# Optimization experiments

Hardware: AMD Instinct MI355X
Metric: run time of the kernel (lower is better)

The kernel has to match this reference:

```python
import jax, jax.numpy as jnp
import numpy as np

MIN_, MAX_, KSZ, IGNORE_IDX = 10, 10, 3, -255
B, H, W = 256, 256, 256
LI_MAX_ITERS = 64


def setup_inputs() -> dict:
    key = jax.random.key(0)
    x = jax.random.uniform(key, (B, 1, H, W), dtype=jnp.float32)
    return {"x": x}


def _otsu(hist):
    # hist: [256] counts. Returns Otsu threshold (bin value); fg = img > t.
    bins = jnp.arange(256, dtype=jnp.float32)
    w0 = jnp.cumsum(hist)[:-1]
    w1 = hist.sum() - w0
    s0 = jnp.cumsum(hist * bins)[:-1]
    s_tot = (hist * bins).sum()
    m0 = s0 / jnp.maximum(w0, 1e-12)
    m1 = (s_tot - s0) / jnp.maximum(w1, 1e-12)
    var_b = w0 * w1 * (m0 - m1) ** 2
    return jnp.argmax(var_b).astype(jnp.float32)


def _li(hist, init_t):
    # Histogram-based Li iterative minimum cross-entropy threshold
    # (skimage.filters.threshold_li with initial_guess=init_t).
    bins = jnp.arange(256, dtype=jnp.float32)
    img_min = jnp.min(jnp.where(hist > 0, bins, 255.0))
    vals = bins - img_min  # shift so values >= 0 (as skimage does)
    csum = jnp.cumsum(hist)
    cvsum = jnp.cumsum(hist * vals)
    n_tot, s_tot = csum[-1], cvsum[-1]
    tol = 0.5  # integer image -> half the minimal value spacing

    def body(state):
        t_curr, _, i = state
        # background: img <= t_curr + img_min
        idx = jnp.clip(jnp.floor(t_curr + img_min).astype(jnp.int32), 0, 255)
        n_back, s_back = csum[idx], cvsum[idx]
        n_fore, s_fore = n_tot - n_back, s_tot - s_back
        mean_back = jnp.where(n_back > 0, s_back / jnp.maximum(n_back, 1.0), 0.0)
        mean_fore = s_fore / jnp.maximum(n_fore, 1.0)
        eps = 1e-12
        t_next = (mean_back - mean_fore) / (
            jnp.log(jnp.maximum(mean_back, eps)) - jnp.log(jnp.maximum(mean_fore, eps)))
        t_next = jnp.where(mean_back < eps, mean_fore / 2.0, t_next)
        return (t_next, t_curr, i + 1)

    def cond(state):
        t_curr, t_prev, i = state
        return (jnp.abs(t_curr - t_prev) > tol) & (i < LI_MAX_ITERS)

    t0 = init_t - img_min
    t_fin, _, _ = jax.lax.while_loop(cond, body, (t0, t0 + 10.0, 0))
    return t_fin + img_min


def _sample_mask(key, region, k):
    # Uniform sampling without replacement of up to k pixels from region
    # (bool [H,W]) via random-score top-k (equiv. to torch.multinomial
    # with uniform probs, w/o replacement).
    flat = region.reshape(-1)
    scores = jnp.where(flat, jax.random.uniform(key, (flat.shape[0],)), -1.0)
    top, idx = jax.lax.top_k(scores, k)
    valid = (top >= 0.0).astype(jnp.int32)
    mask = jnp.zeros(flat.shape[0], jnp.int32).at[idx].max(valid)
    return mask.reshape(region.shape)


def _dilate(m):
    # kornia dilation with ones (KSZ,KSZ) kernel on a 0/1 mask == max filter.
    return jax.lax.reduce_window(m, 0, jax.lax.max, (KSZ, KSZ), (1, 1), "SAME")


def _per_image(img_u8, key_fg, key_bg):
    # img_u8: [H,W] int32 in [0,255]
    hist = jnp.zeros(256, jnp.float32).at[img_u8.ravel()].add(1.0)
    otsu = jnp.clip(_otsu(hist), 1.0, 254.0)  # clamp 0->1, 255->254
    li_t = _li(hist, otsu)
    roi = img_u8.astype(jnp.float32) > li_t

    fg = _sample_mask(key_fg, roi, MAX_)
    bg = _sample_mask(key_bg, jnp.logical_not(roi), MIN_)
    if KSZ > 1:
        fg = _dilate(fg)
        bg = _dilate(bg)

    overlap = (fg + bg) == 2
    fg = jnp.where(overlap, 0, fg)
    bg = jnp.where(overlap, 0, bg)

    seeds = jnp.full((H, W), IGNORE_IDX, jnp.int32)
    seeds = jnp.where(bg == 1, 0, seeds)
    seeds = jnp.where(fg == 1, 1, seeds)
    return seeds


def reference(x):
    b = x.shape[0]
    # (cam*255).astype(uint8): truncation, cam in [0,1]
    img = jnp.clip(jnp.floor(x[:, 0] * 255.0), 0, 255).astype(jnp.int32)
    keys = jax.random.split(jax.random.key(1), (b, 2))
    return jax.vmap(_per_image)(img, keys[:, 0], keys[:, 1])
```

## Files before the change

kernel.cpp:

```cpp
#include <hip/hip_runtime.h>
#include <stdint.h>

#define NPIX 65536
#define IGN (-255)
#define CAP 768

__device__ __forceinline__ uint32_t rotl32(uint32_t v, uint32_t r){
  return __builtin_amdgcn_alignbit(v, v, 32u - r);
}

__device__ __forceinline__ void tf2x32(uint32_t k0, uint32_t k1, uint32_t x0, uint32_t x1,
                                       uint32_t &o0, uint32_t &o1){
  uint32_t k2 = k0 ^ k1 ^ 0x1BD11BDAu;
  x0 += k0; x1 += k1;
#define TFR(r) { x0 += x1; x1 = rotl32(x1,(r)); x1 ^= x0; }
  TFR(13u) TFR(15u) TFR(26u) TFR(6u)   x0 += k1; x1 += k2 + 1u;
  TFR(17u) TFR(29u) TFR(16u) TFR(24u)  x0 += k2; x1 += k0 + 2u;
  TFR(13u) TFR(15u) TFR(26u) TFR(6u)   x0 += k0; x1 += k1 + 3u;
  TFR(17u) TFR(29u) TFR(16u) TFR(24u)  x0 += k1; x1 += k2 + 4u;
  TFR(13u) TFR(15u) TFR(26u) TFR(6u)   x0 += k2; x1 += k0 + 5u;
#undef TFR
  o0 = x0; o1 = x1;
}

__device__ __forceinline__ void tf4_quad(
  uint32_t A0, uint32_t A1, uint32_t A2,
  uint32_t B0, uint32_t B1, uint32_t B2,
  uint32_t C0, uint32_t C1, uint32_t C2,
  uint32_t D0, uint32_t D1, uint32_t D2,
  uint32_t px,
  uint32_t &rA, uint32_t &rB, uint32_t &rC, uint32_t &rD)
{
  uint32_t a0 = A0, a1 = px + A1;
  uint32_t b0 = B0, b1 = (px + 1u) + B1;
  uint32_t c0 = C0, c1 = (px + 2u) + C1;
  uint32_t d0 = D0, d1 = (px + 3u) + D1;
#define R4(r) { a0 += a1; b0 += b1; c0 += c1; d0 += d1;                       \
  a1 = rotl32(a1,(r)); b1 = rotl32(b1,(r)); c1 = rotl32(c1,(r)); d1 = rotl32(d1,(r)); \
  a1 ^= a0; b1 ^= b0; c1 ^= c0; d1 ^= d0; }
#define INJ4(KA,KB,KC,KD, JA,JB,JC,JD, i) {                                   \
  a0 += (KA); b0 += (KB); c0 += (KC); d0 += (KD);                             \
  a1 += (JA) + (i); b1 += (JB) + (i); c1 += (JC) + (i); d1 += (JD) + (i); }
  R4(13u) R4(15u) R4(26u) R4(6u)
  INJ4(A1,B1,C1,D1, A2,B2,C2,D2, 1u)
  R4(17u) R4(29u) R4(16u) R4(24u)
  INJ4(A2,B2,C2,D2, A0,B0,C0,D0, 2u)
  R4(13u) R4(15u) R4(26u) R4(6u)
  INJ4(A0,B0,C0,D0, A1,B1,C1,D1, 3u)
  R4(17u) R4(29u) R4(16u) R4(24u)
  INJ4(A1,B1,C1,D1, A2,B2,C2,D2, 4u)
  R4(13u) R4(15u) R4(26u) R4(6u)
  INJ4(A2,B2,C2,D2, A0,B0,C0,D0, 5u)
#undef R4
#undef INJ4
  rA = a0 ^ a1; rB = b0 ^ b1; rC = c0 ^ c1; rD = d0 ^ d1;
}

__device__ __forceinline__ unsigned long long packCand(uint32_t bits, uint32_t pix){
  float f = __uint_as_float((bits >> 9) | 0x3f800000u) - 1.0f;
  uint32_t u = __float_as_uint(f) ^ 0x80000000u;
  return ((unsigned long long)u << 32) | (unsigned long long)(0xFFFFFFFFu - pix);
}

__device__ __forceinline__ void t10_insert(unsigned long long* l, unsigned long long c){
  if (c > l[9]) {
    l[9] = c;
#pragma unroll
    for (int i = 9; i > 0; --i){
      unsigned long long a = l[i-1], b2 = l[i];
      if (b2 > a){ l[i-1] = b2; l[i] = a; }
    }
  }
}

__global__ __launch_bounds__(1024)
void apm_kernel(const float* __restrict__ x, int* __restrict__ out){
  const int b = blockIdx.x;
  const int tid = threadIdx.x;
  const float* img = x + (size_t)b * NPIX;
  int* outb = out + (size_t)b * NPIX;

  __shared__ uint32_t u8img[16384];
  __shared__ uint32_t histR[1024];
  __shared__ float csum[256], cvsum[256];
  __shared__ uint32_t s_kw[4];
  __shared__ unsigned long long buf[2][CAP];
  __shared__ int s_cnt[2], s_fail[2], s_np[2];
  __shared__ int s_qthr, s_nroi;
  __shared__ unsigned long long s_top[2][64][10];
  __shared__ unsigned long long s_top2[2][8][10];
  __shared__ int s_pr[2][10], s_pc[2][10];

  histR[tid] = 0u;
  if (tid < 2){
    uint32_t o0, o1;
    tf2x32(0u, 1u, 0u, (uint32_t)(2*b + tid), o0, o1);
    s_kw[2*tid] = o0; s_kw[2*tid+1] = o1;
    s_cnt[tid] = 0;
  }
  __syncthreads();

  {
    const float4* x4 = (const float4*)img;
    const uint32_t c4 = (uint32_t)(tid & 3);
#define PROC(V, K) {                                                          \
      uint32_t u0 = (uint32_t)min(max((int)floorf((V).x*255.0f),0),255);      \
      uint32_t u1 = (uint32_t)min(max((int)floorf((V).y*255.0f),0),255);      \
      uint32_t u2 = (uint32_t)min(max((int)floorf((V).z*255.0f),0),255);      \
      uint32_t u3 = (uint32_t)min(max((int)floorf((V).w*255.0f),0),255);      \
      u8img[tid + 1024*(K)] = u0 | (u1<<8) | (u2<<16) | (u3<<24);             \
      atomicAdd(&histR[(u0<<2)|c4],1u); atomicAdd(&histR[(u1<<2)|c4],1u);     \
      atomicAdd(&histR[(u2<<2)|c4],1u); atomicAdd(&histR[(u3<<2)|c4],1u); }
    for (int kk = 0; kk < 2; ++kk){
      int base = 8*kk;
      float4 v0 = x4[tid + 1024*(base+0)];
      float4 v1 = x4[tid + 1024*(base+1)];
      float4 v2 = x4[tid + 1024*(base+2)];
      float4 v3 = x4[tid + 1024*(base+3)];
      float4 v4 = x4[tid + 1024*(base+4)];
      float4 v5 = x4[tid + 1024*(base+5)];
      float4 v6 = x4[tid + 1024*(base+6)];
      float4 v7 = x4[tid + 1024*(base+7)];
      PROC(v0, base+0) PROC(v1, base+1) PROC(v2, base+2) PROC(v3, base+3)
      PROC(v4, base+4) PROC(v5, base+5) PROC(v6, base+6) PROC(v7, base+7)
    }
#undef PROC
  }
  __syncthreads();

  if (tid < 64){
    const int lane = tid;
    const int4* hv = (const int4*)&histR[16*lane];
    int4 p0 = hv[0], p1 = hv[1], p2 = hv[2], p3 = hv[3];
    int h0 = p0.x + p0.y + p0.z + p0.w;
    int h1 = p1.x + p1.y + p1.z + p1.w;
    int h2 = p2.x + p2.y + p2.z + p2.w;
    int h3 = p3.x + p3.y + p3.z + p3.w;
    int cand = 256;
    if (h3) cand = 4*lane + 3;
    if (h2) cand = 4*lane + 2;
    if (h1) cand = 4*lane + 1;
    if (h0) cand = 4*lane + 0;
    for (int off = 32; off; off >>= 1) cand = min(cand, __shfl_xor(cand, off));
    const float img_min = (float)cand;
    float c0 = (float)h0, c1 = c0 + h1, c2 = c1 + h2, c3 = c2 + h3;
    float bv = 4.0f*lane - img_min;
    float v0 = h0*bv;
    float v1 = v0 + h1*(bv + 1.0f);
    float v2 = v1 + h2*(bv + 2.0f);
    float v3 = v2 + h3*(bv + 3.0f);
    float cc = c3, vv = v3;
    for (int off = 1; off < 64; off <<= 1){
      float a = __shfl_up(cc, off), b2 = __shfl_up(vv, off);
      if (lane >= off){ cc += a; vv += b2; }
    }
    const float cexc = cc - c3, vexc = vv - v3;
    const float cs0 = cexc+c0, cs1 = cexc+c1, cs2 = cexc+c2, cs3 = cexc+c3;
    const float vs0 = vexc+v0, vs1 = vexc+v1, vs2 = vexc+v2, vs3 = vexc+v3;
    csum[4*lane]   = cs0; csum[4*lane+1]  = cs1;
    csum[4*lane+2] = cs2; csum[4*lane+3]  = cs3;
    cvsum[4*lane]   = vs0; cvsum[4*lane+1] = vs1;
    cvsum[4*lane+2] = vs2; cvsum[4*lane+3] = vs3;
    const float ctot = __shfl(cc, 63), vtot = __shfl(vv, 63);
    const float s_tot_o = vtot + img_min * ctot;
    unsigned long long best = 0ull;
#define OTSU_BIN(CS, VS, J)                                              \
    { int bin = 4*lane + (J);                                            \
      if (bin < 255){                                                    \
        float w0_ = (CS);                                                \
        float w1_ = 65536.0f - w0_;                                      \
        float cs = (VS) + img_min * (CS);                                \
        float m0 = cs / fmaxf(w0_, 1e-12f);                              \
        float m1 = (s_tot_o - cs) / fmaxf(w1_, 1e-12f);                  \
        float d = m0 - m1;                                               \
        float vb = (w0_*w1_) * (d*d);                                    \
        unsigned long long pk =                                          \
          ((unsigned long long)__float_as_uint(vb) << 32) |              \
           (unsigned long long)(255 - bin);                              \
        if (pk > best) best = pk;                                        \
      } }
    OTSU_BIN(cs0, vs0, 0) OTSU_BIN(cs1, vs1, 1)
    OTSU_BIN(cs2, vs2, 2) OTSU_BIN(cs3, vs3, 3)
#undef OTSU_BIN
    for (int off = 32; off; off >>= 1){
      unsigned int hi = (unsigned int)(best >> 32), lo = (unsigned int)best;
      unsigned int hio = (unsigned int)__shfl_xor((int)hi, off);
      unsigned int loo = (unsigned int)__shfl_xor((int)lo, off);
      unsigned long long ob = ((unsigned long long)hio << 32) | loo;
      if (ob > best) best = ob;
    }
    if (lane == 0){
      int bestIdx = 255 - (int)(best & 0xFFFFFFFFull);
      float otsu = fminf(fmaxf((float)bestIdx, 1.0f), 254.0f);
      float n_tot = ctot, s_tot = vtot;
      float t_curr = otsu - img_min, t_prev = t_curr + 10.0f;
      int it = 0;
      while (fabsf(t_curr - t_prev) > 0.5f && it < 64){
        int idx = min(max((int)floorf(t_curr + img_min), 0), 255);
        float n_back = csum[idx], s_back = cvsum[idx];
        float n_fore = n_tot - n_back, s_fore = s_tot - s_back;
        float mean_back = (n_back > 0.0f) ? (s_back / fmaxf(n_back, 1.0f)) : 0.0f;
        float mean_fore = s_fore / fmaxf(n_fore, 1.0f);
        float t_next = (mean_back - mean_fore) /
                       (logf(fmaxf(mean_back, 1e-12f)) - logf(fmaxf(mean_fore, 1e-12f)));
        if (mean_back < 1e-12f) t_next = mean_fore * 0.5f;
        t_prev = t_curr; t_curr = t_next; ++it;
      }
      float lit = t_curr + img_min;
      int qthr;
      if (!(lit == lit)) qthr = 256;
      else               qthr = (int)floorf(lit) + 1;
      s_qthr = qthr;
      int nlo = (qthr <= 0) ? 0 : (int)csum[min(qthr, 256) - 1];
      s_nroi = NPIX - nlo;
    }
  }
  __syncthreads();

  {
    int4* o4 = (int4*)outb;
    const int4 f4 = make_int4(IGN, IGN, IGN, IGN);
#pragma unroll
    for (int k = 0; k < 16; ++k) o4[tid + 1024*k] = f4;
  }

  const int qthr = s_qthr;
  const uint32_t fk0 = s_kw[0], fk1 = s_kw[1], bk0 = s_kw[2], bk1 = s_kw[3];
  const uint32_t fk2 = fk0 ^ fk1 ^ 0x1BD11BDAu;
  const uint32_t bk2 = bk0 ^ bk1 ^ 0x1BD11BDAu;
  const int4* u4 = (const int4*)u8img;
  for (int k = 0; k < 4; ++k){
    int4 w = u4[tid + 1024*k];
    uint32_t pw0 = (uint32_t)(16*(tid + 1024*k));
#pragma unroll
    for (int m = 0; m < 4; ++m){
      uint32_t pk = (m==0)?(uint32_t)w.x:(m==1)?(uint32_t)w.y:(m==2)?(uint32_t)w.z:(uint32_t)w.w;
      uint32_t pb = pw0 + (uint32_t)(4*m);
      bool r0 = ((int)( pk        & 255u) >= qthr);
      bool r1 = ((int)((pk >>  8) & 255u) >= qthr);
      bool r2 = ((int)((pk >> 16) & 255u) >= qthr);
      bool r3 = ((int)( pk >> 24        ) >= qthr);
      uint32_t bA, bB, bC, bD;
      tf4_quad(r0?fk0:bk0, r0?fk1:bk1, r0?fk2:bk2,
               r1?fk0:bk0, r1?fk1:bk1, r1?fk2:bk2,
               r2?fk0:bk0, r2?fk1:bk1, r2?fk2:bk2,
               r3?fk0:bk0, r3?fk1:bk1, r3?fk2:bk2,
               pb, bA, bB, bC, bD);
#define HIT(BITS, RR, PIX) if ((BITS) >= 0xFF000000u){                        \
        int r2_ = (RR) ? 0 : 1;                                               \
        int idx = atomicAdd(&s_cnt[r2_], 1);                                  \
        if (idx < CAP) buf[r2_][idx] = packCand((BITS), (PIX)); }
      HIT(bA, r0, pb)
      HIT(bB, r1, pb + 1u)
      HIT(bC, r2, pb + 2u)
      HIT(bD, r3, pb + 3u)
#undef HIT
    }
  }
  __syncthreads();

  if (tid < 2){
    int rs = tid ? (NPIX - s_nroi) : s_nroi;
    int cc = s_cnt[tid];
    s_fail[tid] = (cc > CAP) || (cc < 10 && cc != rs);
  }
  __syncthreads();

  const int wv = tid >> 6, lane = tid & 63;
  if (wv < 2){
    const int r2 = wv;
    unsigned long long t[10];
#pragma unroll
    for (int i = 0; i < 10; ++i) t[i] = 0ull;
    if (!s_fail[r2]){
      int n = min(s_cnt[r2], CAP);
      for (int i = lane; i < n; i += 64) t10_insert(t, buf[r2][i]);
    } else {
      const uint32_t kk0 = s_kw[2*r2], kk1 = s_kw[2*r2+1];
      for (int k = 0; k < 1024; ++k){
        uint32_t pix = (uint32_t)(lane + 64*k);
        int q = (int)((u8img[pix >> 2] >> (8*(pix & 3u))) & 255u);
        bool r = (q >= qthr);
        if (r == (r2 == 0)){
          uint32_t o0, o1; tf2x32(kk0, kk1, 0u, pix, o0, o1);
          t10_insert(t, packCand(o0 ^ o1, pix));
        }
      }
    }
#pragma unroll
    for (int i = 0; i < 10; ++i) s_top[r2][lane][i] = t[i];
  }
  __syncthreads();
  if (wv < 2 && lane < 8){
    unsigned long long t[10];
#pragma unroll
    for (int i = 0; i < 10; ++i) t[i] = 0ull;
    for (int l2 = 0; l2 < 8; ++l2)
#pragma unroll
      for (int i = 0; i < 10; ++i) t10_insert(t, s_top[wv][lane*8 + l2][i]);
#pragma unroll
    for (int i = 0; i < 10; ++i) s_top2[wv][lane][i] = t[i];
  }
  __syncthreads();
  if (wv < 2 && lane == 0){
    unsigned long long t[10];
#pragma unroll
    for (int i = 0; i < 10; ++i) t[i] = 0ull;
    for (int l2 = 0; l2 < 8; ++l2)
#pragma unroll
      for (int i = 0; i < 10; ++i) t10_insert(t, s_top2[wv][l2][i]);
    int np = 0;
    for (int i = 0; i < 10; ++i){
      if (t[i]){
        uint32_t pix = 0xFFFFFFFFu - (uint32_t)(t[i] & 0xFFFFFFFFull);
        s_pr[wv][np] = (int)(pix >> 8);
        s_pc[wv][np] = (int)(pix & 255u);
        ++np;
      }
    }
    s_np[wv] = np;
  }
  __syncthreads();

  const int nfg = s_np[0], nbg = s_np[1];
  const int npts = nfg + nbg;
  if (tid < npts*9){
    int k = tid / 9, d = tid - k*9;
    int pr = (k < nfg) ? s_pr[0][k] : s_pr[1][k - nfg];
    int pc = (k < nfg) ? s_pc[0][k] : s_pc[1][k - nfg];
    pr += d/3 - 1; pc += d%3 - 1;
    if (pr >= 0 && pr < 256 && pc >= 0 && pc < 256){
      bool fgd = false, bgd = false;
      for (int i = 0; i < nfg; ++i) fgd |= (abs(pr - s_pr[0][i]) <= 1) && (abs(pc - s_pc[0][i]) <= 1);
      for (int i = 0; i < nbg; ++i) bgd |= (abs(pr - s_pr[1][i]) <= 1) && (abs(pc - s_pc[1][i]) <= 1);
      int val = (fgd && bgd) ? IGN : (fgd ? 1 : 0);
      outb[pr*256 + pc] = val;
    }
  }
}

extern "C" void kernel_launch(void* const* d_in, const int* in_sizes, int n_in,
                              void* d_out, int out_size, void* d_ws, size_t ws_size,
                              hipStream_t stream) {
  const float* x = (const float*)d_in[0];
  int* out = (int*)d_out;
  int B = in_sizes[0] / NPIX;
  apm_kernel<<<B, 1024, 0, stream>>>(x, out);
}
```

Measured before the change: 163.5 us.

## Precompute fixed-key threefry hits before thresholding and filter them by ROI afterwards

Sampling hashes are now computed with fixed fg and bg keys, independent of the Li threshold. The fg hashes are folded into the image load/histogram loop and the bg hashes run right after it, alongside the early IGNORE fill of the output. Candidates are stored as 32-bit pixel indices in per-class buffers, compacted against the ROI once the threshold is known, and their scores are recomputed later with scalar threefry. This removes the per-pixel key selects and moves hashing off the post-threshold critical path, but it doubles the total threefry work and adds an extra compaction pass.

```diff
diff --git a/kernel.cpp b/kernel.cpp
--- a/kernel.cpp
+++ b/kernel.cpp
@@ -3,7 +3,7 @@
 
 #define NPIX 65536
 #define IGN (-255)
-#define CAP 768
+#define HCAP 512
 
 __device__ __forceinline__ uint32_t rotl32(uint32_t v, uint32_t r){
   return __builtin_amdgcn_alignbit(v, v, 32u - r);
@@ -23,36 +23,26 @@
   o0 = x0; o1 = x1;
 }
 
-__device__ __forceinline__ void tf4_quad(
-  uint32_t A0, uint32_t A1, uint32_t A2,
-  uint32_t B0, uint32_t B1, uint32_t B2,
-  uint32_t C0, uint32_t C1, uint32_t C2,
-  uint32_t D0, uint32_t D1, uint32_t D2,
-  uint32_t px,
-  uint32_t &rA, uint32_t &rB, uint32_t &rC, uint32_t &rD)
-{
-  uint32_t a0 = A0, a1 = px + A1;
-  uint32_t b0 = B0, b1 = (px + 1u) + B1;
-  uint32_t c0 = C0, c1 = (px + 2u) + C1;
-  uint32_t d0 = D0, d1 = (px + 3u) + D1;
+__device__ __forceinline__ void tf4_fixed(uint32_t K0, uint32_t K1, uint32_t K2,
+                                          uint32_t px,
+                                          uint32_t &rA, uint32_t &rB,
+                                          uint32_t &rC, uint32_t &rD){
+  uint32_t a0 = K0, a1 = px + K1;
+  uint32_t b0 = K0, b1 = (px + 1u) + K1;
+  uint32_t c0 = K0, c1 = (px + 2u) + K1;
+  uint32_t d0 = K0, d1 = (px + 3u) + K1;
 #define R4(r) { a0 += a1; b0 += b1; c0 += c1; d0 += d1;                       \
   a1 = rotl32(a1,(r)); b1 = rotl32(b1,(r)); c1 = rotl32(c1,(r)); d1 = rotl32(d1,(r)); \
   a1 ^= a0; b1 ^= b0; c1 ^= c0; d1 ^= d0; }
-#define INJ4(KA,KB,KC,KD, JA,JB,JC,JD, i) {                                   \
-  a0 += (KA); b0 += (KB); c0 += (KC); d0 += (KD);                             \
-  a1 += (JA) + (i); b1 += (JB) + (i); c1 += (JC) + (i); d1 += (JD) + (i); }
-  R4(13u) R4(15u) R4(26u) R4(6u)
-  INJ4(A1,B1,C1,D1, A2,B2,C2,D2, 1u)
-  R4(17u) R4(29u) R4(16u) R4(24u)
-  INJ4(A2,B2,C2,D2, A0,B0,C0,D0, 2u)
-  R4(13u) R4(15u) R4(26u) R4(6u)
-  INJ4(A0,B0,C0,D0, A1,B1,C1,D1, 3u)
-  R4(17u) R4(29u) R4(16u) R4(24u)
-  INJ4(A1,B1,C1,D1, A2,B2,C2,D2, 4u)
-  R4(13u) R4(15u) R4(26u) R4(6u)
-  INJ4(A2,B2,C2,D2, A0,B0,C0,D0, 5u)
+#define I4(K, J, i) { a0 += (K); b0 += (K); c0 += (K); d0 += (K);             \
+  a1 += (J) + (i); b1 += (J) + (i); c1 += (J) + (i); d1 += (J) + (i); }
+  R4(13u) R4(15u) R4(26u) R4(6u)   I4(K1, K2, 1u)
+  R4(17u) R4(29u) R4(16u) R4(24u)  I4(K2, K0, 2u)
+  R4(13u) R4(15u) R4(26u) R4(6u)   I4(K0, K1, 3u)
+  R4(17u) R4(29u) R4(16u) R4(24u)  I4(K1, K2, 4u)
+  R4(13u) R4(15u) R4(26u) R4(6u)   I4(K2, K0, 5u)
 #undef R4
-#undef INJ4
+#undef I4
   rA = a0 ^ a1; rB = b0 ^ b1; rC = c0 ^ c1; rD = d0 ^ d1;
 }
 
@@ -84,8 +74,8 @@
   __shared__ uint32_t histR[1024];
   __shared__ float csum[256], cvsum[256];
   __shared__ uint32_t s_kw[4];
-  __shared__ unsigned long long buf[2][CAP];
-  __shared__ int s_cnt[2], s_fail[2], s_np[2];
+  __shared__ int bufF[HCAP], bufB[HCAP];
+  __shared__ int s_hc[2], s_cc[2], s_fail[2], s_np[2];
   __shared__ int s_qthr, s_nroi;
   __shared__ unsigned long long s_top[2][64][10];
   __shared__ unsigned long long s_top2[2][8][10];
@@ -96,9 +86,13 @@
     uint32_t o0, o1;
     tf2x32(0u, 1u, 0u, (uint32_t)(2*b + tid), o0, o1);
     s_kw[2*tid] = o0; s_kw[2*tid+1] = o1;
-    s_cnt[tid] = 0;
-  }
-  __syncthreads();
+    s_hc[tid] = 0; s_cc[tid] = 0;
+  }
+  __syncthreads();
+
+  const uint32_t fk0 = s_kw[0], fk1 = s_kw[1], bk0 = s_kw[2], bk1 = s_kw[3];
+  const uint32_t fk2 = fk0 ^ fk1 ^ 0x1BD11BDAu;
+  const uint32_t bk2 = bk0 ^ bk1 ^ 0x1BD11BDAu;
 
   {
     const float4* x4 = (const float4*)img;
@@ -110,23 +104,42 @@
       uint32_t u3 = (uint32_t)min(max((int)floorf((V).w*255.0f),0),255);      \
       u8img[tid + 1024*(K)] = u0 | (u1<<8) | (u2<<16) | (u3<<24);             \
       atomicAdd(&histR[(u0<<2)|c4],1u); atomicAdd(&histR[(u1<<2)|c4],1u);     \
-      atomicAdd(&histR[(u2<<2)|c4],1u); atomicAdd(&histR[(u3<<2)|c4],1u); }
-    for (int kk = 0; kk < 2; ++kk){
-      int base = 8*kk;
+      atomicAdd(&histR[(u2<<2)|c4],1u); atomicAdd(&histR[(u3<<2)|c4],1u);     \
+      uint32_t pb = (uint32_t)(4*(tid + 1024*(K)));                           \
+      uint32_t hA,hB,hC,hD;                                                   \
+      tf4_fixed(fk0,fk1,fk2, pb, hA,hB,hC,hD);                                \
+      if (hA >= 0xFF000000u){ int i2=atomicAdd(&s_hc[0],1); if(i2<HCAP) bufF[i2]=(int)pb; }      \
+      if (hB >= 0xFF000000u){ int i2=atomicAdd(&s_hc[0],1); if(i2<HCAP) bufF[i2]=(int)(pb+1u); } \
+      if (hC >= 0xFF000000u){ int i2=atomicAdd(&s_hc[0],1); if(i2<HCAP) bufF[i2]=(int)(pb+2u); } \
+      if (hD >= 0xFF000000u){ int i2=atomicAdd(&s_hc[0],1); if(i2<HCAP) bufF[i2]=(int)(pb+3u); } }
+    for (int kk = 0; kk < 4; ++kk){
+      int base = 4*kk;
       float4 v0 = x4[tid + 1024*(base+0)];
       float4 v1 = x4[tid + 1024*(base+1)];
       float4 v2 = x4[tid + 1024*(base+2)];
       float4 v3 = x4[tid + 1024*(base+3)];
-      float4 v4 = x4[tid + 1024*(base+4)];
-      float4 v5 = x4[tid + 1024*(base+5)];
-      float4 v6 = x4[tid + 1024*(base+6)];
-      float4 v7 = x4[tid + 1024*(base+7)];
       PROC(v0, base+0) PROC(v1, base+1) PROC(v2, base+2) PROC(v3, base+3)
-      PROC(v4, base+4) PROC(v5, base+5) PROC(v6, base+6) PROC(v7, base+7)
     }
 #undef PROC
   }
   __syncthreads();
+
+  {
+    int4* o4 = (int4*)outb;
+    const int4 f4 = make_int4(IGN, IGN, IGN, IGN);
+#pragma unroll
+    for (int k = 0; k < 16; ++k) o4[tid + 1024*k] = f4;
+  }
+
+  for (int k = 0; k < 16; ++k){
+    uint32_t pb = (uint32_t)(4*(tid + 1024*k));
+    uint32_t hA,hB,hC,hD;
+    tf4_fixed(bk0,bk1,bk2, pb, hA,hB,hC,hD);
+    if (hA >= 0xFF000000u){ int i2=atomicAdd(&s_hc[1],1); if(i2<HCAP) bufB[i2]=(int)pb; }
+    if (hB >= 0xFF000000u){ int i2=atomicAdd(&s_hc[1],1); if(i2<HCAP) bufB[i2]=(int)(pb+1u); }
+    if (hC >= 0xFF000000u){ int i2=atomicAdd(&s_hc[1],1); if(i2<HCAP) bufB[i2]=(int)(pb+2u); }
+    if (hD >= 0xFF000000u){ int i2=atomicAdd(&s_hc[1],1); if(i2<HCAP) bufB[i2]=(int)(pb+3u); }
+  }
 
   if (tid < 64){
     const int lane = tid;
@@ -217,52 +230,25 @@
   }
   __syncthreads();
 
+  const int qthr = s_qthr;
   {
-    int4* o4 = (int4*)outb;
-    const int4 f4 = make_int4(IGN, IGN, IGN, IGN);
-#pragma unroll
-    for (int k = 0; k < 16; ++k) o4[tid + 1024*k] = f4;
-  }
-
-  const int qthr = s_qthr;
-  const uint32_t fk0 = s_kw[0], fk1 = s_kw[1], bk0 = s_kw[2], bk1 = s_kw[3];
-  const uint32_t fk2 = fk0 ^ fk1 ^ 0x1BD11BDAu;
-  const uint32_t bk2 = bk0 ^ bk1 ^ 0x1BD11BDAu;
-  const int4* u4 = (const int4*)u8img;
-  for (int k = 0; k < 4; ++k){
-    int4 w = u4[tid + 1024*k];
-    uint32_t pw0 = (uint32_t)(16*(tid + 1024*k));
-#pragma unroll
-    for (int m = 0; m < 4; ++m){
-      uint32_t pk = (m==0)?(uint32_t)w.x:(m==1)?(uint32_t)w.y:(m==2)?(uint32_t)w.z:(uint32_t)w.w;
-      uint32_t pb = pw0 + (uint32_t)(4*m);
-      bool r0 = ((int)( pk        & 255u) >= qthr);
-      bool r1 = ((int)((pk >>  8) & 255u) >= qthr);
-      bool r2 = ((int)((pk >> 16) & 255u) >= qthr);
-      bool r3 = ((int)( pk >> 24        ) >= qthr);
-      uint32_t bA, bB, bC, bD;
-      tf4_quad(r0?fk0:bk0, r0?fk1:bk1, r0?fk2:bk2,
-               r1?fk0:bk0, r1?fk1:bk1, r1?fk2:bk2,
-               r2?fk0:bk0, r2?fk1:bk1, r2?fk2:bk2,
-               r3?fk0:bk0, r3?fk1:bk1, r3?fk2:bk2,
-               pb, bA, bB, bC, bD);
-#define HIT(BITS, RR, PIX) if ((BITS) >= 0xFF000000u){                        \
-        int r2_ = (RR) ? 0 : 1;                                               \
-        int idx = atomicAdd(&s_cnt[r2_], 1);                                  \
-        if (idx < CAP) buf[r2_][idx] = packCand((BITS), (PIX)); }
-      HIT(bA, r0, pb)
-      HIT(bB, r1, pb + 1u)
-      HIT(bC, r2, pb + 2u)
-      HIT(bD, r3, pb + 3u)
-#undef HIT
-    }
+    int rawF = min(s_hc[0], HCAP), rawB = min(s_hc[1], HCAP);
+    int pF = -1, pB = -1;
+    if (tid < rawF) pF = bufF[tid];
+    if (tid < rawB) pB = bufB[tid];
+    bool kF = (pF >= 0) &&
+      ((int)((u8img[(uint32_t)pF >> 2] >> (8*((uint32_t)pF & 3u))) & 255u) >= qthr);
+    bool kB = (pB >= 0) &&
+      ((int)((u8img[(uint32_t)pB >> 2] >> (8*((uint32_t)pB & 3u))) & 255u) <  qthr);
+    __syncthreads();
+    if (kF){ int i2 = atomicAdd(&s_cc[0], 1); bufF[i2] = pF; }
+    if (kB){ int i2 = atomicAdd(&s_cc[1], 1); bufB[i2] = pB; }
   }
   __syncthreads();
 
   if (tid < 2){
     int rs = tid ? (NPIX - s_nroi) : s_nroi;
-    int cc = s_cnt[tid];
-    s_fail[tid] = (cc > CAP) || (cc < 10 && cc != rs);
+    s_fail[tid] = (s_hc[tid] > HCAP) || (s_cc[tid] < 10 && s_cc[tid] != rs);
   }
   __syncthreads();
 
@@ -272,11 +258,16 @@
     unsigned long long t[10];
 #pragma unroll
     for (int i = 0; i < 10; ++i) t[i] = 0ull;
+    const uint32_t kk0 = s_kw[2*r2], kk1 = s_kw[2*r2+1];
     if (!s_fail[r2]){
-      int n = min(s_cnt[r2], CAP);
-      for (int i = lane; i < n; i += 64) t10_insert(t, buf[r2][i]);
+      int n = s_cc[r2];
+      const int* cl = r2 ? bufB : bufF;
+      for (int i = lane; i < n; i += 64){
+        uint32_t pix = (uint32_t)cl[i];
+        uint32_t o0, o1; tf2x32(kk0, kk1, 0u, pix, o0, o1);
+        t10_insert(t, packCand(o0 ^ o1, pix));
+      }
     } else {
-      const uint32_t kk0 = s_kw[2*r2], kk1 = s_kw[2*r2+1];
       for (int k = 0; k < 1024; ++k){
         uint32_t pix = (uint32_t)(lane + 64*k);
         int q = (int)((u8img[pix >> 2] >> (8*(pix & 3u))) & 255u);
```

Result: slower. 190.2 us (+16.3%).
